# Performance work log

Measured on AMD Instinct MI355X. Metric: run time of the kernel, lower is better.

Reference implementation:

```python
import jax, jax.numpy as jnp
import numpy as np

N_NODES = 50000
HIDDEN = 128
N_EDGES = 1_600_000


def gcn_conv(x, W, b, src, dst, n_nodes):
    """PyG GCNConv: linear, add self-loops, symmetric deg^-1/2 normalization, scatter-sum."""
    h = x @ W  # [N, D]
    # degree with self-loops: 1 + in-degree from edges (edge weight 1)
    deg = jnp.ones((n_nodes,), h.dtype).at[dst].add(1.0)
    dinv = jax.lax.rsqrt(deg)  # deg^{-1/2}, deg >= 1 so no inf
    # neighbor messages: norm_e = dinv[src] * dinv[dst]
    msgs = h[src] * (dinv[src] * dinv[dst])[:, None]  # [E, D]
    agg = jnp.zeros_like(h).at[dst].add(msgs)
    # self-loop contribution: norm = dinv[i]*dinv[i]
    agg = agg + h * (dinv * dinv)[:, None]
    return agg + b


def setup_inputs() -> dict:
    key = jax.random.key(0)
    ks = jax.random.split(key, 7)
    x = jax.random.normal(ks[0], (N_NODES, HIDDEN), dtype=jnp.float32)
    edge_index = jax.random.randint(ks[1], (2, N_EDGES), 0, N_NODES, dtype=jnp.int64)
    s = 1.0 / np.sqrt(HIDDEN)
    W1 = jax.random.uniform(ks[2], (HIDDEN, HIDDEN), jnp.float32, -s, s)
    b1 = jax.random.uniform(ks[3], (HIDDEN,), jnp.float32, -s, s)
    W2 = jax.random.uniform(ks[4], (HIDDEN, HIDDEN), jnp.float32, -s, s)
    b2 = jax.random.uniform(ks[5], (HIDDEN,), jnp.float32, -s, s)
    return {"x": x, "edge_index": edge_index, "W1": W1, "b1": b1, "W2": W2, "b2": b2}


def reference(x, edge_index, W1, b1, W2, b2):
    src, dst = edge_index[0], edge_index[1]
    h = jax.nn.relu(gcn_conv(x, W1, b1, src, dst, N_NODES))
    z = gcn_conv(h, W2, b2, src, dst, N_NODES)
    return z
```

## Files before the change

### kernel.cpp

```cpp
#include <hip/hip_runtime.h>
#include <hip/hip_fp16.h>
#include <type_traits>

#define D 128
#define NI 128
#define NR 12500

using half8 = __attribute__((ext_vector_type(8))) _Float16;
using f32x4 = __attribute__((ext_vector_type(4))) float;


__global__ __launch_bounds__(256) void wprep_kernel(const float* __restrict__ W1,
                                                    const float* __restrict__ W2,
                                                    __half* __restrict__ Wt1,
                                                    __half* __restrict__ Wt2) {
  const float* W = blockIdx.x ? W2 : W1;
  __half* Wt = blockIdx.x ? Wt2 : Wt1;
  for (int idx = threadIdx.x; idx < D * D; idx += 256) {
    int c = idx & 127, k = idx >> 7;
    Wt[c * D + k] = __float2half(W[k * D + c]);
  }
}


__global__ __launch_bounds__(1024) void histA_kernel(const int* __restrict__ dst,
                                                     unsigned short* __restrict__ c,
                                                     int E, int N, int CH) {
  __shared__ int cnt[NR];
  int i = blockIdx.x, r = blockIdx.y;
  int base = r * NR;
  int kmax = min(NR, N - base);
  for (int k = threadIdx.x; k < kmax; k += 1024) cnt[k] = 0;
  __syncthreads();
  int e0 = i * CH, e1 = min(e0 + CH, E);
  for (int e = e0 + (int)threadIdx.x; e < e1; e += 1024) {
    unsigned dr = (unsigned)(dst[e] - base);
    if (dr < (unsigned)kmax) atomicAdd(&cnt[dr], 1);
  }
  __syncthreads();
  unsigned short* ci = c + (size_t)i * N + base;
  for (int k = threadIdx.x; k < kmax; k += 1024) ci[k] = (unsigned short)cnt[k];
}


__global__ __launch_bounds__(256) void histB_kernel(unsigned short* __restrict__ c,
                                                    int* __restrict__ deg, int N) {
  int n = blockIdx.x * 256 + threadIdx.x;
  if (n >= N) return;
  int run = 0;
  #pragma unroll 8
  for (int i = 0; i < NI; ++i) {
    size_t idx = (size_t)i * N + n;
    int v = c[idx];
    c[idx] = (unsigned short)run;
    run += v;
  }
  deg[n] = run;
}


__global__ __launch_bounds__(256) void bsum_kernel(const int* __restrict__ deg,
                                                   int* __restrict__ bsum) {
  __shared__ int ws[4];
  int i0 = blockIdx.x * 1024 + threadIdx.x * 4;
  int4 v = *reinterpret_cast<const int4*>(deg + i0);
  int s = v.x + v.y + v.z + v.w;
  #pragma unroll
  for (int off = 32; off; off >>= 1) s += __shfl_down(s, off);
  if ((threadIdx.x & 63) == 0) ws[threadIdx.x >> 6] = s;
  __syncthreads();
  if (threadIdx.x == 0) bsum[blockIdx.x] = ws[0] + ws[1] + ws[2] + ws[3];
}


__global__ __launch_bounds__(256) void scan_kernel(const int* __restrict__ deg,
                                                   const int* __restrict__ bsum,
                                                   int* __restrict__ offsets,
                                                   float* __restrict__ dinv,
                                                   int N, int E) {
  __shared__ int ts[256];
  int b = blockIdx.x;
  int base = 0;
  for (int t = 0; t < b; ++t) base += bsum[t];

  int i0 = b * 1024 + threadIdx.x * 4;
  int4 v = *reinterpret_cast<const int4*>(deg + i0);
  int t4 = v.x + v.y + v.z + v.w;
  ts[threadIdx.x] = t4;
  __syncthreads();
  #pragma unroll
  for (int off = 1; off < 256; off <<= 1) {
    int u = (threadIdx.x >= off) ? ts[threadIdx.x - off] : 0;
    __syncthreads();
    ts[threadIdx.x] += u;
    __syncthreads();
  }
  int run = base + ts[threadIdx.x] - t4;

  int dd[4] = {v.x, v.y, v.z, v.w};
  #pragma unroll
  for (int k = 0; k < 4; ++k) {
    int i = i0 + k;
    if (i < N) {
      offsets[i] = run;
      dinv[i] = rsqrtf(1.0f + (float)dd[k]);
    }
    run += dd[k];
  }
  if (b == 0 && threadIdx.x == 0) offsets[N] = E;
}


__global__ __launch_bounds__(1024) void placeC_kernel(const int* __restrict__ src,
                                                      const int* __restrict__ dst,
                                                      const unsigned short* __restrict__ c,
                                                      const int* __restrict__ offsets,
                                                      const float* __restrict__ dinv,
                                                      unsigned int* __restrict__ csr,
                                                      int E, int N, int CH) {
  __shared__ int cnt[NR];
  int i = blockIdx.x, r = blockIdx.y;
  int base = r * NR;
  int kmax = min(NR, N - base);
  const unsigned short* ci = c + (size_t)i * N + base;
  for (int k = threadIdx.x; k < kmax; k += 1024) cnt[k] = offsets[base + k] + (int)ci[k];
  __syncthreads();
  int e0 = i * CH, e1 = min(e0 + CH, E);
  for (int e = e0 + (int)threadIdx.x; e < e1; e += 1024) {
    int d = dst[e];
    unsigned dr = (unsigned)(d - base);
    if (dr < (unsigned)kmax) {
      int pos = atomicAdd(&cnt[dr], 1);
      int s = src[e];
      float nm = dinv[s] * dinv[d];
      unsigned int q = (unsigned int)__float2int_rn(nm * 32767.0f);
      csr[pos] = ((unsigned int)s << 15) | q;
    }
  }
}


template <typename TI>
__global__ __launch_bounds__(256) void gemm_mfma_kernel(const TI* __restrict__ X,
                                                        const __half* __restrict__ Wt,
                                                        __half* __restrict__ H, int N) {
  int wid = threadIdx.x >> 6;
  int l = threadIdx.x & 63;
  int row0w = blockIdx.x * 64 + wid * 16;
  int arow = row0w + (l & 15);
  int k0 = (l >> 4) * 8;

  half8 A[4];
  #pragma unroll
  for (int kt = 0; kt < 4; ++kt) {
    half8 a = {};
    if (arow < N) {
      if constexpr (std::is_same<TI, float>::value) {
        const float* p = X + (size_t)arow * D + kt * 32 + k0;
        float4 u = *reinterpret_cast<const float4*>(p);
        float4 v = *reinterpret_cast<const float4*>(p + 4);
        a[0] = (_Float16)u.x; a[1] = (_Float16)u.y;
        a[2] = (_Float16)u.z; a[3] = (_Float16)u.w;
        a[4] = (_Float16)v.x; a[5] = (_Float16)v.y;
        a[6] = (_Float16)v.z; a[7] = (_Float16)v.w;
      } else {
        a = *reinterpret_cast<const half8*>((const __half*)X + (size_t)arow * D + kt * 32 + k0);
      }
    }
    A[kt] = a;
  }

  int wrow = row0w + (l >> 4) * 4;
  int col = l & 15;
  #pragma unroll
  for (int ct = 0; ct < 8; ++ct) {
    f32x4 acc = {0.f, 0.f, 0.f, 0.f};
    #pragma unroll
    for (int kt = 0; kt < 4; ++kt) {
      half8 b = *reinterpret_cast<const half8*>(Wt + (size_t)(ct * 16 + col) * D + kt * 32 + k0);
      acc = __builtin_amdgcn_mfma_f32_16x16x32_f16(A[kt], b, acc, 0, 0, 0);
    }
    #pragma unroll
    for (int r = 0; r < 4; ++r) {
      int row = wrow + r;
      if (row < N) H[(size_t)row * D + ct * 16 + col] = __float2half(acc[r]);
    }
  }
}


template <int DO_RELU, typename TO>
__global__ __launch_bounds__(256) void agg_kernel(const __half* __restrict__ H,
                                                  const int* __restrict__ offsets,
                                                  const unsigned int* __restrict__ csr,
                                                  const float* __restrict__ dinv,
                                                  const float* __restrict__ bias,
                                                  TO* __restrict__ out, int N) {
  int n = blockIdx.x * 4 + (threadIdx.x >> 6);
  if (n >= N) return;
  int lane = threadIdx.x & 63;
  int g = lane >> 4;
  int l = lane & 15;

  int beg = offsets[n];
  int end = offsets[n + 1];

  float acc[8];
  #pragma unroll
  for (int k = 0; k < 8; ++k) acc[k] = 0.f;

  const __half* Hl = H + l * 8;

  int j = beg + g;
  for (; j + 12 < end; j += 16) {
    unsigned int p0 = csr[j];
    unsigned int p1 = csr[j + 4];
    unsigned int p2 = csr[j + 8];
    unsigned int p3 = csr[j + 12];
    float m0 = (float)(p0 & 0x7fffu) * (1.0f / 32767.0f);
    float m1 = (float)(p1 & 0x7fffu) * (1.0f / 32767.0f);
    float m2 = (float)(p2 & 0x7fffu) * (1.0f / 32767.0f);
    float m3 = (float)(p3 & 0x7fffu) * (1.0f / 32767.0f);
    uint4 r0 = *reinterpret_cast<const uint4*>(Hl + (size_t)(p0 >> 15) * D);
    uint4 r1 = *reinterpret_cast<const uint4*>(Hl + (size_t)(p1 >> 15) * D);
    uint4 r2 = *reinterpret_cast<const uint4*>(Hl + (size_t)(p2 >> 15) * D);
    uint4 r3 = *reinterpret_cast<const uint4*>(Hl + (size_t)(p3 >> 15) * D);
    const __half2* h0 = reinterpret_cast<const __half2*>(&r0);
    const __half2* h1 = reinterpret_cast<const __half2*>(&r1);
    const __half2* h2 = reinterpret_cast<const __half2*>(&r2);
    const __half2* h3 = reinterpret_cast<const __half2*>(&r3);
    #pragma unroll
    for (int k = 0; k < 4; ++k) {
      float2 f0 = __half22float2(h0[k]);
      float2 f1 = __half22float2(h1[k]);
      float2 f2 = __half22float2(h2[k]);
      float2 f3 = __half22float2(h3[k]);
      acc[2 * k]     = fmaf(f0.x, m0, acc[2 * k]);
      acc[2 * k + 1] = fmaf(f0.y, m0, acc[2 * k + 1]);
      acc[2 * k]     = fmaf(f1.x, m1, acc[2 * k]);
      acc[2 * k + 1] = fmaf(f1.y, m1, acc[2 * k + 1]);
      acc[2 * k]     = fmaf(f2.x, m2, acc[2 * k]);
      acc[2 * k + 1] = fmaf(f2.y, m2, acc[2 * k + 1]);
      acc[2 * k]     = fmaf(f3.x, m3, acc[2 * k]);
      acc[2 * k + 1] = fmaf(f3.y, m3, acc[2 * k + 1]);
    }
  }
  for (; j < end; j += 4) {
    unsigned int p0 = csr[j];
    float m0 = (float)(p0 & 0x7fffu) * (1.0f / 32767.0f);
    uint4 r0 = *reinterpret_cast<const uint4*>(Hl + (size_t)(p0 >> 15) * D);
    const __half2* h0 = reinterpret_cast<const __half2*>(&r0);
    #pragma unroll
    for (int k = 0; k < 4; ++k) {
      float2 f0 = __half22float2(h0[k]);
      acc[2 * k]     = fmaf(f0.x, m0, acc[2 * k]);
      acc[2 * k + 1] = fmaf(f0.y, m0, acc[2 * k + 1]);
    }
  }

  #pragma unroll
  for (int k = 0; k < 8; ++k) {
    acc[k] += __shfl_xor(acc[k], 16);
    acc[k] += __shfl_xor(acc[k], 32);
  }

  if (g == 0) {
    float di = dinv[n];
    float dii = di * di;
    uint4 rs = *reinterpret_cast<const uint4*>(Hl + (size_t)n * D);
    const __half2* hs = reinterpret_cast<const __half2*>(&rs);
    float4 bv0 = *reinterpret_cast<const float4*>(bias + l * 8);
    float4 bv1 = *reinterpret_cast<const float4*>(bias + l * 8 + 4);
    float v[8];
    #pragma unroll
    for (int k = 0; k < 4; ++k) {
      float2 f = __half22float2(hs[k]);
      v[2 * k]     = fmaf(f.x, dii, acc[2 * k]);
      v[2 * k + 1] = fmaf(f.y, dii, acc[2 * k + 1]);
    }
    v[0] += bv0.x; v[1] += bv0.y; v[2] += bv0.z; v[3] += bv0.w;
    v[4] += bv1.x; v[5] += bv1.y; v[6] += bv1.z; v[7] += bv1.w;
    if (DO_RELU) {
      #pragma unroll
      for (int k = 0; k < 8; ++k) v[k] = fmaxf(v[k], 0.f);
    }
    if constexpr (std::is_same<TO, float>::value) {
      float4 o0 = make_float4(v[0], v[1], v[2], v[3]);
      float4 o1 = make_float4(v[4], v[5], v[6], v[7]);
      *reinterpret_cast<float4*>(out + (size_t)n * D + l * 8) = o0;
      *reinterpret_cast<float4*>(out + (size_t)n * D + l * 8 + 4) = o1;
    } else {
      uint4 pk;
      __half2 q0 = __floats2half2_rn(v[0], v[1]);
      __half2 q1 = __floats2half2_rn(v[2], v[3]);
      __half2 q2 = __floats2half2_rn(v[4], v[5]);
      __half2 q3 = __floats2half2_rn(v[6], v[7]);
      pk.x = *reinterpret_cast<unsigned int*>(&q0);
      pk.y = *reinterpret_cast<unsigned int*>(&q1);
      pk.z = *reinterpret_cast<unsigned int*>(&q2);
      pk.w = *reinterpret_cast<unsigned int*>(&q3);
      *reinterpret_cast<uint4*>((__half*)out + (size_t)n * D + l * 8) = pk;
    }
  }
}


extern "C" void kernel_launch(void* const* d_in, const int* in_sizes, int n_in,
                              void* d_out, int out_size, void* d_ws, size_t ws_size,
                              hipStream_t stream) {
  const float* x  = (const float*)d_in[0];
  const int* edge = (const int*)d_in[1];
  const float* W1 = (const float*)d_in[2];
  const float* b1 = (const float*)d_in[3];
  const float* W2 = (const float*)d_in[4];
  const float* b2 = (const float*)d_in[5];
  const int N = in_sizes[0] / D;
  const int E = in_sizes[1] / 2;
  const int* srcp = edge;
  const int* dstp = edge + E;
  float* out = (float*)d_out;

  const int NP = (N + 1023) & ~1023;
  const int SB = NP / 1024;
  const int CH = (E + NI - 1) / NI;
  const int NRB = (N + NR - 1) / NR;

  auto align = [](size_t v) { return (v + 255) & ~(size_t)255; };
  char* ws = (char*)d_ws;
  size_t o = 0;
  int*   deg     = (int*)(ws + o);             o += align((size_t)NP * 4);
  int*   bsum    = (int*)(ws + o);             o += align((size_t)SB * 4);
  int*   offsets = (int*)(ws + o);             o += align((size_t)(N + 1) * 4);
  float* dinv    = (float*)(ws + o);           o += align((size_t)N * 4);
  unsigned short* c = (unsigned short*)(ws + o); o += align((size_t)NI * N * 2);
  unsigned int* csr = (unsigned int*)(ws + o); o += align((size_t)E * 4);
  __half* Hh     = (__half*)(ws + o);          o += align((size_t)N * D * 2);
  __half* h1h    = (__half*)(ws + o);          o += align((size_t)N * D * 2);
  __half* Wt1    = (__half*)(ws + o);          o += align((size_t)D * D * 2);
  __half* Wt2    = (__half*)(ws + o);          o += align((size_t)D * D * 2);

  int gemm_blocks = (N + 63) / 64;
  int agg_blocks  = (N + 3) / 4;

  hipMemsetAsync(deg, 0, (size_t)NP * 4, stream);
  wprep_kernel<<<2, 256, 0, stream>>>(W1, W2, Wt1, Wt2);
  histA_kernel<<<dim3(NI, NRB), 1024, 0, stream>>>(dstp, c, E, N, CH);
  histB_kernel<<<(N + 255) / 256, 256, 0, stream>>>(c, deg, N);
  bsum_kernel<<<SB, 256, 0, stream>>>(deg, bsum);
  scan_kernel<<<SB, 256, 0, stream>>>(deg, bsum, offsets, dinv, N, E);
  placeC_kernel<<<dim3(NI, NRB), 1024, 0, stream>>>(srcp, dstp, c, offsets, dinv, csr, E, N, CH);

  gemm_mfma_kernel<float><<<gemm_blocks, 256, 0, stream>>>(x, Wt1, Hh, N);
  agg_kernel<1, __half><<<agg_blocks, 256, 0, stream>>>(Hh, offsets, csr, dinv, b1, h1h, N);

  gemm_mfma_kernel<__half><<<gemm_blocks, 256, 0, stream>>>(h1h, Wt2, Hh, N);
  agg_kernel<0, float><<<agg_blocks, 256, 0, stream>>>(Hh, offsets, csr, dinv, b2, out, N);
}
```

Baseline: 233.9 us.

## Record per-edge ranks in histogram and place CSR edges without atomics

The histogram kernel now packs two 16-bit node counters per shared-memory word so that all nodes fit in one block's LDS. Each edge's rank within its chunk is recorded as the atomic's return value, which removes the dst-range split across blocks. Placement becomes a fully parallel, atomic-free kernel that computes each edge's CSR slot from offsets, the chunk prefix count and the rank. The per-edge weight stores only dinv[src], and the aggregation applies dinv[dst] once per node. This adds a rank buffer, and 16-bit per-chunk counts could overflow if any node receives 65536 or more edges within one chunk.

```diff
diff --git a/kernel.cpp b/kernel.cpp
--- a/kernel.cpp
+++ b/kernel.cpp
@@ -3,8 +3,8 @@
 #include <type_traits>
 
 #define D 128
-#define NI 128
-#define NR 12500
+#define NI 256
+#define MAXNW 25024
 
 using half8 = __attribute__((ext_vector_type(8))) _Float16;
 using f32x4 = __attribute__((ext_vector_type(4))) float;
@@ -25,21 +25,33 @@
 
 __global__ __launch_bounds__(1024) void histA_kernel(const int* __restrict__ dst,
                                                      unsigned short* __restrict__ c,
+                                                     unsigned short* __restrict__ rank,
                                                      int E, int N, int CH) {
-  __shared__ int cnt[NR];
-  int i = blockIdx.x, r = blockIdx.y;
-  int base = r * NR;
-  int kmax = min(NR, N - base);
-  for (int k = threadIdx.x; k < kmax; k += 1024) cnt[k] = 0;
+  __shared__ unsigned int cnt[MAXNW];
+  int i = blockIdx.x;
+  int nw = (N + 1) >> 1;
+  for (int k = threadIdx.x; k < nw; k += 1024) cnt[k] = 0u;
   __syncthreads();
   int e0 = i * CH, e1 = min(e0 + CH, E);
   for (int e = e0 + (int)threadIdx.x; e < e1; e += 1024) {
-    unsigned dr = (unsigned)(dst[e] - base);
-    if (dr < (unsigned)kmax) atomicAdd(&cnt[dr], 1);
+    int d = dst[e];
+    int sh = (d & 1) * 16;
+    unsigned int old = atomicAdd(&cnt[d >> 1], 1u << sh);
+    rank[e] = (unsigned short)((old >> sh) & 0xffffu);
   }
   __syncthreads();
-  unsigned short* ci = c + (size_t)i * N + base;
-  for (int k = threadIdx.x; k < kmax; k += 1024) ci[k] = (unsigned short)cnt[k];
+  unsigned short* ci = c + (size_t)i * N;
+  if ((N & 1) == 0) {
+    unsigned int* ci32 = reinterpret_cast<unsigned int*>(ci);
+    for (int k = threadIdx.x; k < nw; k += 1024) ci32[k] = cnt[k];
+  } else {
+    for (int k = threadIdx.x; k < nw; k += 1024) {
+      unsigned int v = cnt[k];
+      int n0 = k * 2;
+      ci[n0] = (unsigned short)(v & 0xffffu);
+      if (n0 + 1 < N) ci[n0 + 1] = (unsigned short)(v >> 16);
+    }
+  }
 }
 
 
@@ -111,29 +123,44 @@
 }
 
 
-__global__ __launch_bounds__(1024) void placeC_kernel(const int* __restrict__ src,
-                                                      const int* __restrict__ dst,
-                                                      const unsigned short* __restrict__ c,
-                                                      const int* __restrict__ offsets,
-                                                      const float* __restrict__ dinv,
-                                                      unsigned int* __restrict__ csr,
-                                                      int E, int N, int CH) {
-  __shared__ int cnt[NR];
-  int i = blockIdx.x, r = blockIdx.y;
-  int base = r * NR;
-  int kmax = min(NR, N - base);
-  const unsigned short* ci = c + (size_t)i * N + base;
-  for (int k = threadIdx.x; k < kmax; k += 1024) cnt[k] = offsets[base + k] + (int)ci[k];
-  __syncthreads();
-  int e0 = i * CH, e1 = min(e0 + CH, E);
-  for (int e = e0 + (int)threadIdx.x; e < e1; e += 1024) {
-    int d = dst[e];
-    unsigned dr = (unsigned)(d - base);
-    if (dr < (unsigned)kmax) {
-      int pos = atomicAdd(&cnt[dr], 1);
+__global__ __launch_bounds__(256) void place_kernel(const int* __restrict__ src,
+                                                    const int* __restrict__ dst,
+                                                    const unsigned short* __restrict__ rank,
+                                                    const unsigned short* __restrict__ c,
+                                                    const int* __restrict__ offsets,
+                                                    const float* __restrict__ dinv,
+                                                    unsigned int* __restrict__ csr,
+                                                    int E, int N, int CH) {
+  int t = blockIdx.x * 256 + threadIdx.x;
+  int e0 = t * 4;
+  if (e0 + 4 <= E) {
+    int4 s4 = *reinterpret_cast<const int4*>(src + e0);
+    int4 d4 = *reinterpret_cast<const int4*>(dst + e0);
+    ushort4 r4 = *reinterpret_cast<const ushort4*>(rank + e0);
+    int ss[4] = {s4.x, s4.y, s4.z, s4.w};
+    int dd[4] = {d4.x, d4.y, d4.z, d4.w};
+    int rr[4] = {r4.x, r4.y, r4.z, r4.w};
+    int pos[4];
+    float w[4];
+    #pragma unroll
+    for (int k = 0; k < 4; ++k) {
+      int i = (e0 + k) / CH;
+      pos[k] = offsets[dd[k]] + (int)c[(size_t)i * N + dd[k]] + rr[k];
+    }
+    #pragma unroll
+    for (int k = 0; k < 4; ++k) w[k] = dinv[ss[k]];
+    #pragma unroll
+    for (int k = 0; k < 4; ++k) {
+      unsigned int q = (unsigned int)__float2int_rn(w[k] * 32767.0f);
+      csr[pos[k]] = ((unsigned int)ss[k] << 15) | q;
+    }
+  } else {
+    for (int e = e0; e < E; ++e) {
       int s = src[e];
-      float nm = dinv[s] * dinv[d];
-      unsigned int q = (unsigned int)__float2int_rn(nm * 32767.0f);
+      int d = dst[e];
+      int i = e / CH;
+      int pos = offsets[d] + (int)c[(size_t)i * N + d] + (int)rank[e];
+      unsigned int q = (unsigned int)__float2int_rn(dinv[s] * 32767.0f);
       csr[pos] = ((unsigned int)s << 15) | q;
     }
   }
@@ -266,7 +293,6 @@
 
   if (g == 0) {
     float di = dinv[n];
-    float dii = di * di;
     uint4 rs = *reinterpret_cast<const uint4*>(Hl + (size_t)n * D);
     const __half2* hs = reinterpret_cast<const __half2*>(&rs);
     float4 bv0 = *reinterpret_cast<const float4*>(bias + l * 8);
@@ -275,8 +301,8 @@
     #pragma unroll
     for (int k = 0; k < 4; ++k) {
       float2 f = __half22float2(hs[k]);
-      v[2 * k]     = fmaf(f.x, dii, acc[2 * k]);
-      v[2 * k + 1] = fmaf(f.y, dii, acc[2 * k + 1]);
+      v[2 * k]     = fmaf(di, fmaf(di, f.x, acc[2 * k]), 0.f);
+      v[2 * k + 1] = fmaf(di, fmaf(di, f.y, acc[2 * k + 1]), 0.f);
     }
     v[0] += bv0.x; v[1] += bv0.y; v[2] += bv0.z; v[3] += bv0.w;
     v[4] += bv1.x; v[5] += bv1.y; v[6] += bv1.z; v[7] += bv1.w;
@@ -323,7 +349,6 @@
   const int NP = (N + 1023) & ~1023;
   const int SB = NP / 1024;
   const int CH = (E + NI - 1) / NI;
-  const int NRB = (N + NR - 1) / NR;
 
   auto align = [](size_t v) { return (v + 255) & ~(size_t)255; };
   char* ws = (char*)d_ws;
@@ -332,7 +357,8 @@
   int*   bsum    = (int*)(ws + o);             o += align((size_t)SB * 4);
   int*   offsets = (int*)(ws + o);             o += align((size_t)(N + 1) * 4);
   float* dinv    = (float*)(ws + o);           o += align((size_t)N * 4);
-  unsigned short* c = (unsigned short*)(ws + o); o += align((size_t)NI * N * 2);
+  unsigned short* c    = (unsigned short*)(ws + o); o += align((size_t)NI * N * 2);
+  unsigned short* rank = (unsigned short*)(ws + o); o += align((size_t)((E + 3) & ~3) * 2);
   unsigned int* csr = (unsigned int*)(ws + o); o += align((size_t)E * 4);
   __half* Hh     = (__half*)(ws + o);          o += align((size_t)N * D * 2);
   __half* h1h    = (__half*)(ws + o);          o += align((size_t)N * D * 2);
@@ -344,11 +370,13 @@
 
   hipMemsetAsync(deg, 0, (size_t)NP * 4, stream);
   wprep_kernel<<<2, 256, 0, stream>>>(W1, W2, Wt1, Wt2);
-  histA_kernel<<<dim3(NI, NRB), 1024, 0, stream>>>(dstp, c, E, N, CH);
+  histA_kernel<<<NI, 1024, 0, stream>>>(dstp, c, rank, E, N, CH);
   histB_kernel<<<(N + 255) / 256, 256, 0, stream>>>(c, deg, N);
   bsum_kernel<<<SB, 256, 0, stream>>>(deg, bsum);
   scan_kernel<<<SB, 256, 0, stream>>>(deg, bsum, offsets, dinv, N, E);
-  placeC_kernel<<<dim3(NI, NRB), 1024, 0, stream>>>(srcp, dstp, c, offsets, dinv, csr, E, N, CH);
+  int pl_threads = (E + 3) / 4;
+  place_kernel<<<(pl_threads + 255) / 256, 256, 0, stream>>>(srcp, dstp, rank, c, offsets,
+                                                             dinv, csr, E, N, CH);
 
   gemm_mfma_kernel<float><<<gemm_blocks, 256, 0, stream>>>(x, Wt1, Hh, N);
   agg_kernel<1, __half><<<agg_blocks, 256, 0, stream>>>(Hh, offsets, csr, dinv, b1, h1h, N);
```

After: 265.0 us. +13.3%, slower.

## Fuse weight prep into histogram kernel, shrink node ranges, drop memset

Applied to the files above, without the earlier changes.

Folds the weight transpose/convert kernel into the histogram launch as two extra blocks and removes the deg memset by having histB zero the padding entries. This cuts two launches from the graph. The node-range partition goes from 4 ranges of 12500 to 8 ranges of 6250 with 512-thread blocks, so there are twice as many blocks and each uses less shared memory. Each thread now handles 4 contiguous edges per iteration, which changes the memory access pattern and means each thread reads dst 8 times over all ranges instead of 4. NRB is hardcoded to 8, which assumes N at most 50000.

```diff
diff --git a/kernel.cpp b/kernel.cpp
--- a/kernel.cpp
+++ b/kernel.cpp
@@ -4,49 +4,56 @@
 
 #define D 128
 #define NI 128
-#define NR 12500
+#define NRB 8
+#define NR 6250
 
 using half8 = __attribute__((ext_vector_type(8))) _Float16;
 using f32x4 = __attribute__((ext_vector_type(4))) float;
 
 
-__global__ __launch_bounds__(256) void wprep_kernel(const float* __restrict__ W1,
+__global__ __launch_bounds__(512) void histA_kernel(const int* __restrict__ dst,
+                                                    unsigned short* __restrict__ c,
+                                                    const float* __restrict__ W1,
                                                     const float* __restrict__ W2,
                                                     __half* __restrict__ Wt1,
-                                                    __half* __restrict__ Wt2) {
-  const float* W = blockIdx.x ? W2 : W1;
-  __half* Wt = blockIdx.x ? Wt2 : Wt1;
-  for (int idx = threadIdx.x; idx < D * D; idx += 256) {
-    int c = idx & 127, k = idx >> 7;
-    Wt[c * D + k] = __float2half(W[k * D + c]);
-  }
-}
-
-
-__global__ __launch_bounds__(1024) void histA_kernel(const int* __restrict__ dst,
-                                                     unsigned short* __restrict__ c,
-                                                     int E, int N, int CH) {
+                                                    __half* __restrict__ Wt2,
+                                                    int E, int N, int CH) {
+  int L = blockIdx.x;
+  if (L >= NI * NRB) {
+    const float* W = (L - NI * NRB) ? W2 : W1;
+    __half* Wt = (L - NI * NRB) ? Wt2 : Wt1;
+    for (int idx = threadIdx.x; idx < D * D; idx += 512) {
+      int cc = idx & 127, k = idx >> 7;
+      Wt[cc * D + k] = __float2half(W[k * D + cc]);
+    }
+    return;
+  }
   __shared__ int cnt[NR];
-  int i = blockIdx.x, r = blockIdx.y;
+  int r = L & 7, i = L >> 3;
   int base = r * NR;
   int kmax = min(NR, N - base);
-  for (int k = threadIdx.x; k < kmax; k += 1024) cnt[k] = 0;
+  for (int k = threadIdx.x; k < kmax; k += 512) cnt[k] = 0;
   __syncthreads();
   int e0 = i * CH, e1 = min(e0 + CH, E);
-  for (int e = e0 + (int)threadIdx.x; e < e1; e += 1024) {
-    unsigned dr = (unsigned)(dst[e] - base);
-    if (dr < (unsigned)kmax) atomicAdd(&cnt[dr], 1);
+  for (int eb = e0 + (int)threadIdx.x * 4; eb < e1; eb += 2048) {
+    int ee = min(eb + 4, e1);
+    #pragma unroll 4
+    for (int e = eb; e < ee; ++e) {
+      unsigned dr = (unsigned)(dst[e] - base);
+      if (dr < (unsigned)kmax) atomicAdd(&cnt[dr], 1);
+    }
   }
   __syncthreads();
   unsigned short* ci = c + (size_t)i * N + base;
-  for (int k = threadIdx.x; k < kmax; k += 1024) ci[k] = (unsigned short)cnt[k];
+  for (int k = threadIdx.x; k < kmax; k += 512) ci[k] = (unsigned short)cnt[k];
 }
 
 
 __global__ __launch_bounds__(256) void histB_kernel(unsigned short* __restrict__ c,
-                                                    int* __restrict__ deg, int N) {
+                                                    int* __restrict__ deg, int N, int NP) {
   int n = blockIdx.x * 256 + threadIdx.x;
-  if (n >= N) return;
+  if (n >= NP) return;
+  if (n >= N) { deg[n] = 0; return; }
   int run = 0;
   #pragma unroll 8
   for (int i = 0; i < NI; ++i) {
@@ -111,30 +118,35 @@
 }
 
 
-__global__ __launch_bounds__(1024) void placeC_kernel(const int* __restrict__ src,
-                                                      const int* __restrict__ dst,
-                                                      const unsigned short* __restrict__ c,
-                                                      const int* __restrict__ offsets,
-                                                      const float* __restrict__ dinv,
-                                                      unsigned int* __restrict__ csr,
-                                                      int E, int N, int CH) {
+__global__ __launch_bounds__(512) void placeC_kernel(const int* __restrict__ src,
+                                                     const int* __restrict__ dst,
+                                                     const unsigned short* __restrict__ c,
+                                                     const int* __restrict__ offsets,
+                                                     const float* __restrict__ dinv,
+                                                     unsigned int* __restrict__ csr,
+                                                     int E, int N, int CH) {
   __shared__ int cnt[NR];
-  int i = blockIdx.x, r = blockIdx.y;
+  int L = blockIdx.x;
+  int r = L & 7, i = L >> 3;
   int base = r * NR;
   int kmax = min(NR, N - base);
   const unsigned short* ci = c + (size_t)i * N + base;
-  for (int k = threadIdx.x; k < kmax; k += 1024) cnt[k] = offsets[base + k] + (int)ci[k];
+  for (int k = threadIdx.x; k < kmax; k += 512) cnt[k] = offsets[base + k] + (int)ci[k];
   __syncthreads();
   int e0 = i * CH, e1 = min(e0 + CH, E);
-  for (int e = e0 + (int)threadIdx.x; e < e1; e += 1024) {
-    int d = dst[e];
-    unsigned dr = (unsigned)(d - base);
-    if (dr < (unsigned)kmax) {
-      int pos = atomicAdd(&cnt[dr], 1);
-      int s = src[e];
-      float nm = dinv[s] * dinv[d];
-      unsigned int q = (unsigned int)__float2int_rn(nm * 32767.0f);
-      csr[pos] = ((unsigned int)s << 15) | q;
+  for (int eb = e0 + (int)threadIdx.x * 4; eb < e1; eb += 2048) {
+    int ee = min(eb + 4, e1);
+    #pragma unroll 4
+    for (int e = eb; e < ee; ++e) {
+      int d = dst[e];
+      unsigned dr = (unsigned)(d - base);
+      if (dr < (unsigned)kmax) {
+        int pos = atomicAdd(&cnt[dr], 1);
+        int s = src[e];
+        float nm = dinv[s] * dinv[d];
+        unsigned int q = (unsigned int)__float2int_rn(nm * 32767.0f);
+        csr[pos] = ((unsigned int)s << 15) | q;
+      }
     }
   }
 }
@@ -323,7 +335,6 @@
   const int NP = (N + 1023) & ~1023;
   const int SB = NP / 1024;
   const int CH = (E + NI - 1) / NI;
-  const int NRB = (N + NR - 1) / NR;
 
   auto align = [](size_t v) { return (v + 255) & ~(size_t)255; };
   char* ws = (char*)d_ws;
@@ -342,13 +353,11 @@
   int gemm_blocks = (N + 63) / 64;
   int agg_blocks  = (N + 3) / 4;
 
-  hipMemsetAsync(deg, 0, (size_t)NP * 4, stream);
-  wprep_kernel<<<2, 256, 0, stream>>>(W1, W2, Wt1, Wt2);
-  histA_kernel<<<dim3(NI, NRB), 1024, 0, stream>>>(dstp, c, E, N, CH);
-  histB_kernel<<<(N + 255) / 256, 256, 0, stream>>>(c, deg, N);
+  histA_kernel<<<NI * NRB + 2, 512, 0, stream>>>(dstp, c, W1, W2, Wt1, Wt2, E, N, CH);
+  histB_kernel<<<(NP + 255) / 256, 256, 0, stream>>>(c, deg, N, NP);
   bsum_kernel<<<SB, 256, 0, stream>>>(deg, bsum);
   scan_kernel<<<SB, 256, 0, stream>>>(deg, bsum, offsets, dinv, N, E);
-  placeC_kernel<<<dim3(NI, NRB), 1024, 0, stream>>>(srcp, dstp, c, offsets, dinv, csr, E, N, CH);
+  placeC_kernel<<<NI * NRB, 512, 0, stream>>>(srcp, dstp, c, offsets, dinv, csr, E, N, CH);
 
   gemm_mfma_kernel<float><<<gemm_blocks, 256, 0, stream>>>(x, Wt1, Hh, N);
   agg_kernel<1, __half><<<agg_blocks, 256, 0, stream>>>(Hh, offsets, csr, dinv, b1, h1h, N);
```

New measurement: 248.9 us. 6.4% more time.

## Retune histogram and placement node-range partitions, drop deg memset

Applied to the files above, without the earlier changes.

The histogram kernel now uses larger node ranges (25000 nodes, 2 range blocks) so each edge chunk is scanned fewer times. The placement kernel uses smaller ranges (6250 nodes, 8 ranges) with 512-thread blocks, a flattened grid ordered with range fastest, and 4 consecutive edges per thread. The deg memset is replaced by histB zero-filling the padding entries. The aim is to cut redundant edge rereads in histA and raise occupancy and locality in placeC. In exchange, placeC rereads the edge arrays more times, and its strided per-thread access may hurt coalescing.

```diff
diff --git a/kernel.cpp b/kernel.cpp
--- a/kernel.cpp
+++ b/kernel.cpp
@@ -4,7 +4,8 @@
 
 #define D 128
 #define NI 128
-#define NR 12500
+#define NRA 25000
+#define NRC 6250
 
 using half8 = __attribute__((ext_vector_type(8))) _Float16;
 using f32x4 = __attribute__((ext_vector_type(4))) float;
@@ -26,10 +27,10 @@
 __global__ __launch_bounds__(1024) void histA_kernel(const int* __restrict__ dst,
                                                      unsigned short* __restrict__ c,
                                                      int E, int N, int CH) {
-  __shared__ int cnt[NR];
+  __shared__ int cnt[NRA];
   int i = blockIdx.x, r = blockIdx.y;
-  int base = r * NR;
-  int kmax = min(NR, N - base);
+  int base = r * NRA;
+  int kmax = min(NRA, N - base);
   for (int k = threadIdx.x; k < kmax; k += 1024) cnt[k] = 0;
   __syncthreads();
   int e0 = i * CH, e1 = min(e0 + CH, E);
@@ -44,9 +45,10 @@
 
 
 __global__ __launch_bounds__(256) void histB_kernel(unsigned short* __restrict__ c,
-                                                    int* __restrict__ deg, int N) {
+                                                    int* __restrict__ deg, int N, int NP) {
   int n = blockIdx.x * 256 + threadIdx.x;
-  if (n >= N) return;
+  if (n >= NP) return;
+  if (n >= N) { deg[n] = 0; return; }
   int run = 0;
   #pragma unroll 8
   for (int i = 0; i < NI; ++i) {
@@ -111,30 +113,35 @@
 }
 
 
-__global__ __launch_bounds__(1024) void placeC_kernel(const int* __restrict__ src,
-                                                      const int* __restrict__ dst,
-                                                      const unsigned short* __restrict__ c,
-                                                      const int* __restrict__ offsets,
-                                                      const float* __restrict__ dinv,
-                                                      unsigned int* __restrict__ csr,
-                                                      int E, int N, int CH) {
-  __shared__ int cnt[NR];
-  int i = blockIdx.x, r = blockIdx.y;
-  int base = r * NR;
-  int kmax = min(NR, N - base);
+__global__ __launch_bounds__(512) void placeC_kernel(const int* __restrict__ src,
+                                                     const int* __restrict__ dst,
+                                                     const unsigned short* __restrict__ c,
+                                                     const int* __restrict__ offsets,
+                                                     const float* __restrict__ dinv,
+                                                     unsigned int* __restrict__ csr,
+                                                     int E, int N, int CH) {
+  __shared__ int cnt[NRC];
+  int L = blockIdx.x;
+  int r = L & 7, i = L >> 3;
+  int base = r * NRC;
+  int kmax = min(NRC, N - base);
   const unsigned short* ci = c + (size_t)i * N + base;
-  for (int k = threadIdx.x; k < kmax; k += 1024) cnt[k] = offsets[base + k] + (int)ci[k];
+  for (int k = threadIdx.x; k < kmax; k += 512) cnt[k] = offsets[base + k] + (int)ci[k];
   __syncthreads();
   int e0 = i * CH, e1 = min(e0 + CH, E);
-  for (int e = e0 + (int)threadIdx.x; e < e1; e += 1024) {
-    int d = dst[e];
-    unsigned dr = (unsigned)(d - base);
-    if (dr < (unsigned)kmax) {
-      int pos = atomicAdd(&cnt[dr], 1);
-      int s = src[e];
-      float nm = dinv[s] * dinv[d];
-      unsigned int q = (unsigned int)__float2int_rn(nm * 32767.0f);
-      csr[pos] = ((unsigned int)s << 15) | q;
+  for (int eb = e0 + (int)threadIdx.x * 4; eb < e1; eb += 2048) {
+    int ee = min(eb + 4, e1);
+    #pragma unroll 4
+    for (int e = eb; e < ee; ++e) {
+      int d = dst[e];
+      unsigned dr = (unsigned)(d - base);
+      if (dr < (unsigned)kmax) {
+        int pos = atomicAdd(&cnt[dr], 1);
+        int s = src[e];
+        float nm = dinv[s] * dinv[d];
+        unsigned int q = (unsigned int)__float2int_rn(nm * 32767.0f);
+        csr[pos] = ((unsigned int)s << 15) | q;
+      }
     }
   }
 }
@@ -323,7 +330,8 @@
   const int NP = (N + 1023) & ~1023;
   const int SB = NP / 1024;
   const int CH = (E + NI - 1) / NI;
-  const int NRB = (N + NR - 1) / NR;
+  const int NRBA = (N + NRA - 1) / NRA;
+  const int NRBC = (N + NRC - 1) / NRC;
 
   auto align = [](size_t v) { return (v + 255) & ~(size_t)255; };
   char* ws = (char*)d_ws;
@@ -342,13 +350,12 @@
   int gemm_blocks = (N + 63) / 64;
   int agg_blocks  = (N + 3) / 4;
 
-  hipMemsetAsync(deg, 0, (size_t)NP * 4, stream);
   wprep_kernel<<<2, 256, 0, stream>>>(W1, W2, Wt1, Wt2);
-  histA_kernel<<<dim3(NI, NRB), 1024, 0, stream>>>(dstp, c, E, N, CH);
-  histB_kernel<<<(N + 255) / 256, 256, 0, stream>>>(c, deg, N);
+  histA_kernel<<<dim3(NI, NRBA), 1024, 0, stream>>>(dstp, c, E, N, CH);
+  histB_kernel<<<(NP + 255) / 256, 256, 0, stream>>>(c, deg, N, NP);
   bsum_kernel<<<SB, 256, 0, stream>>>(deg, bsum);
   scan_kernel<<<SB, 256, 0, stream>>>(deg, bsum, offsets, dinv, N, E);
-  placeC_kernel<<<dim3(NI, NRB), 1024, 0, stream>>>(srcp, dstp, c, offsets, dinv, csr, E, N, CH);
+  placeC_kernel<<<NI * NRBC, 512, 0, stream>>>(srcp, dstp, c, offsets, dinv, csr, E, N, CH);
 
   gemm_mfma_kernel<float><<<gemm_blocks, 256, 0, stream>>>(x, Wt1, Hh, N);
   agg_kernel<1, __half><<<agg_blocks, 256, 0, stream>>>(Hh, offsets, csr, dinv, b1, h1h, N);
```

New measurement: 245.7 us. 5.1% more time.
